# Kernel optimization log

Measured on AMD Instinct MI355X. Metric: run time of the kernel, lower is better.

Reference implementation:

```python
import jax, jax.numpy as jnp
import numpy as np

N_NODES = 100000
N_EDGES = 1600000
IN_C = 128
HID_C = 128   # 2 * out_channels
OUT_C = 64


def gcn_conv(x, row, col, w, W, b, num_nodes):
    """PyG GCNConv: linear transform, add self-loops (weight 1),
    symmetric degree normalization, scatter-sum aggregation, bias."""
    h = x @ W  # [N, C_out]
    loop = jnp.arange(num_nodes, dtype=row.dtype)
    r = jnp.concatenate([row, loop])
    c = jnp.concatenate([col, loop])
    ew = jnp.concatenate([w, jnp.ones((num_nodes,), dtype=w.dtype)])
    deg = jax.ops.segment_sum(ew, c, num_segments=num_nodes)
    dinv = jnp.where(deg > 0, jax.lax.rsqrt(deg), 0.0)
    norm = dinv[r] * ew * dinv[c]            # [E+N]
    msg = h[r] * norm[:, None]               # [E+N, C_out] gather
    out = jax.ops.segment_sum(msg, c, num_segments=num_nodes)
    return out + b


def setup_inputs() -> dict:
    key = jax.random.key(0)
    k1, k2, k3, k4, k5, k6, k7, k8 = jax.random.split(key, 8)
    x = jax.random.normal(k1, (N_NODES, IN_C), dtype=jnp.float32)
    edge_index = jax.random.randint(k2, (2, N_EDGES), 0, N_NODES, dtype=jnp.int64)
    edge_weight = jax.random.uniform(k3, (N_EDGES,), dtype=jnp.float32)
    s1 = float(np.sqrt(6.0 / (IN_C + HID_C)))
    s2 = float(np.sqrt(6.0 / (HID_C + OUT_C)))
    W1 = jax.random.uniform(k4, (IN_C, HID_C), minval=-s1, maxval=s1, dtype=jnp.float32)
    b1 = jnp.zeros((HID_C,), dtype=jnp.float32)
    W2 = jax.random.uniform(k5, (HID_C, OUT_C), minval=-s2, maxval=s2, dtype=jnp.float32)
    b2 = jnp.zeros((OUT_C,), dtype=jnp.float32)
    return {"x": x, "edge_index": edge_index, "edge_weight": edge_weight,
            "W1": W1, "b1": b1, "W2": W2, "b2": b2}


def reference(x, edge_index, edge_weight, W1, b1, W2, b2):
    row, col = edge_index[0], edge_index[1]
    n = x.shape[0]
    h = jax.nn.relu(gcn_conv(x, row, col, edge_weight, W1, b1, n))
    h = jax.nn.relu(gcn_conv(h, row, col, edge_weight, W2, b2, n))
    return h
```

## Files before the change

kernel.cpp:

```cpp
#include <hip/hip_runtime.h>

#define TPB 256

typedef unsigned int uint32;
typedef unsigned short ushort_t;
typedef __attribute__((ext_vector_type(8))) short bf16x8;
typedef __attribute__((ext_vector_type(4))) float f32x4;

constexpr int NB = 256;
constexpr int B1 = 256;

__device__ __forceinline__ uint32 pack_bf16x2(float a, float b) {
  uint32 ua = __float_as_uint(a), ub = __float_as_uint(b);
  ua += 0x7FFFu + ((ua >> 16) & 1u);
  ub += 0x7FFFu + ((ub >> 16) & 1u);
  return (ua >> 16) | (ub & 0xFFFF0000u);
}
__device__ __forceinline__ ushort_t bf16_of(float a) {
  uint32 u = __float_as_uint(a);
  u += 0x7FFFu + ((u >> 16) & 1u);
  return (ushort_t)(u >> 16);
}
__device__ __forceinline__ float bf16_lo(uint32 u) { return __uint_as_float(u << 16); }
__device__ __forceinline__ float bf16_hi(uint32 u) { return __uint_as_float(u & 0xFFFF0000u); }
__device__ __forceinline__ int edge_src(uint32 e) { return (int)(e >> 15); }
__device__ __forceinline__ float edge_w(uint32 e) { return __uint_as_float((e & 0x7FFFu) << 16); }

__global__ __launch_bounds__(256) void rx_hist(const int* __restrict__ col,
                                               int* __restrict__ blockhist, int e, int chunk,
                                               const float* __restrict__ W1, ushort_t* __restrict__ Wt1,
                                               const float* __restrict__ W2, ushort_t* __restrict__ Wt2) {
  __shared__ int h[NB];
  int tid = threadIdx.x, blk = blockIdx.x;
  h[tid] = 0;
  __syncthreads();
  int s = blk * chunk, t = min(e, s + chunk);
  for (int i = s + tid; i < t; i += 256) atomicAdd(&h[col[i] & 255], 1);
  int gtid = blk * 256 + tid;
  if (gtid < 128 * 128) {
    int k = gtid >> 7, m = gtid & 127;
    Wt1[m * 128 + k] = bf16_of(W1[gtid]);
  } else if (gtid < 128 * 128 + 128 * 64) {
    int j = gtid - 128 * 128;
    int k = j >> 6, m = j & 63;
    Wt2[m * 128 + k] = bf16_of(W2[j]);
  }
  __syncthreads();
  blockhist[tid * B1 + blk] = h[tid];
}

__global__ __launch_bounds__(256) void k_scan1(int* __restrict__ a, int* __restrict__ bsum, int n) {
  __shared__ int s[256];
  int tid = threadIdx.x;
  int base = blockIdx.x * 1024 + tid * 4;
  int v0 = 0, v1 = 0, v2 = 0, v3 = 0;
  if (base + 0 < n) v0 = a[base + 0];
  if (base + 1 < n) v1 = a[base + 1];
  if (base + 2 < n) v2 = a[base + 2];
  if (base + 3 < n) v3 = a[base + 3];
  int tsum = v0 + v1 + v2 + v3;
  s[tid] = tsum;
  __syncthreads();
  for (int off = 1; off < 256; off <<= 1) {
    int t = (tid >= off) ? s[tid - off] : 0;
    __syncthreads();
    s[tid] += t;
    __syncthreads();
  }
  if (tid == 255) bsum[blockIdx.x] = s[255];
  int e0 = s[tid] - tsum;
  int e1 = e0 + v0, e2 = e1 + v1, e3 = e2 + v2;
  if (base + 0 < n) a[base + 0] = e0;
  if (base + 1 < n) a[base + 1] = e1;
  if (base + 2 < n) a[base + 2] = e2;
  if (base + 3 < n) a[base + 3] = e3;
}

__global__ __launch_bounds__(256) void k_scan2(int* __restrict__ bsum, int nb) {
  __shared__ int s[256];
  int tid = threadIdx.x;
  int v = (tid < nb) ? bsum[tid] : 0;
  s[tid] = v;
  __syncthreads();
  for (int off = 1; off < 256; off <<= 1) {
    int t = (tid >= off) ? s[tid - off] : 0;
    __syncthreads();
    s[tid] += t;
    __syncthreads();
  }
  if (tid < nb) bsum[tid] = s[tid] - v;
}

__global__ __launch_bounds__(256) void rx_scatter1(const int* __restrict__ row,
                                                   const int* __restrict__ col,
                                                   const float* __restrict__ w,
                                                   const int* __restrict__ scanned,
                                                   const int* __restrict__ bsum,
                                                   int2* __restrict__ rec, int e, int chunk) {
  __shared__ int cur[NB];
  int tid = threadIdx.x, blk = blockIdx.x;
  int idx = tid * B1 + blk;
  cur[tid] = scanned[idx] + bsum[idx >> 10];
  __syncthreads();
  int s = blk * chunk, t = min(e, s + chunk);
  for (int i = s + tid; i < t; i += 256) {
    int c = col[i];
    int p = atomicAdd(&cur[c & 255], 1);
    rec[p] = make_int2(row[i] | ((c >> 8) << 20), __float_as_int(w[i]));
  }
}

__global__ __launch_bounds__(256) void rx_build(const int2* __restrict__ rec,
                                                const int* __restrict__ scanned,
                                                const int* __restrict__ bsum,
                                                int2* __restrict__ nodeRange,
                                                float* __restrict__ dinv,
                                                uint32* __restrict__ edges, int n, int e) {
  constexpr int NH = 512;
  __shared__ int cnt[NH];
  __shared__ int pref[NH];
  __shared__ int cur[NH];
  __shared__ float dw[NH];
  __shared__ int ssum[256];
  int tid = threadIdx.x, lo = blockIdx.x;
  int si = lo * B1;
  int s = scanned[si] + bsum[si >> 10];
  int t;
  if (lo == NB - 1) t = e;
  else {
    int ti = (lo + 1) * B1;
    t = scanned[ti] + bsum[ti >> 10];
  }
  cnt[tid] = 0; cnt[tid + 256] = 0;
  dw[tid] = 0.f; dw[tid + 256] = 0.f;
  __syncthreads();
  for (int i = s + tid; i < t; i += 256) {
    int2 r = rec[i];
    int hi = ((uint32)r.x) >> 20;
    atomicAdd(&cnt[hi], 1);
    atomicAdd(&dw[hi], __int_as_float(r.y));
  }
  __syncthreads();
  int a0 = cnt[2 * tid], a1 = cnt[2 * tid + 1];
  int sum2 = a0 + a1;
  ssum[tid] = sum2;
  __syncthreads();
  for (int off = 1; off < 256; off <<= 1) {
    int v = (tid >= off) ? ssum[tid - off] : 0;
    __syncthreads();
    ssum[tid] += v;
    __syncthreads();
  }
  int excl = ssum[tid] - sum2;
  pref[2 * tid] = excl;
  pref[2 * tid + 1] = excl + a0;
  __syncthreads();
#pragma unroll
  for (int k = 0; k < 2; ++k) {
    int hi = tid + k * 256;
    int node = (hi << 8) | lo;
    cur[hi] = s + pref[hi];
    if (node < n) {
      nodeRange[node] = make_int2(s + pref[hi], cnt[hi]);
      dinv[node] = rsqrtf(1.0f + dw[hi]);
    }
  }
  __syncthreads();
  for (int i = s + tid; i < t; i += 256) {
    int2 r = rec[i];
    int hi = ((uint32)r.x) >> 20;
    int p = atomicAdd(&cur[hi], 1);
    uint32 src = (uint32)(r.x & 0x1FFFF);
    uint32 wb = (uint32)bf16_of(__int_as_float(r.y)) & 0x7FFFu;
    edges[p] = (src << 15) | wb;
  }
}

template <int M, bool XF32>
__global__ __launch_bounds__(256) void k_gemm_mfma(
    const void* __restrict__ Xv, const ushort_t* __restrict__ Wt,
    const float* __restrict__ dinv, uint32* __restrict__ Hb, int n) {
  __shared__ __align__(16) char smem[16384 + M * 256];
  char* Xs = smem;
  char* Ws = smem + 16384;
  const int tid = threadIdx.x;
  const int lane = tid & 63;
  const int w = tid >> 6;
  const int row0 = blockIdx.x * 64;

  {
    const uint4* src = (const uint4*)Wt;
    for (int idx = tid; idx < M * 16; idx += 256) {
      int r = idx >> 4, g = idx & 15;
      uint4 v = src[idx];
      *(uint4*)(Ws + ((r << 8) | ((g << 4) ^ ((r & 7) << 4)))) = v;
    }
  }
  if constexpr (XF32) {
    const float4* src = (const float4*)Xv;
    for (int idx = tid; idx < 64 * 16; idx += 256) {
      int r = idx >> 4, g = idx & 15;
      int grow = row0 + r;
      float4 va = make_float4(0.f, 0.f, 0.f, 0.f), vb = va;
      if (grow < n) {
        va = src[(size_t)grow * 32 + g * 2];
        vb = src[(size_t)grow * 32 + g * 2 + 1];
      }
      uint4 p;
      p.x = pack_bf16x2(va.x, va.y);
      p.y = pack_bf16x2(va.z, va.w);
      p.z = pack_bf16x2(vb.x, vb.y);
      p.w = pack_bf16x2(vb.z, vb.w);
      *(uint4*)(Xs + ((r << 8) | ((g << 4) ^ ((r & 7) << 4)))) = p;
    }
  } else {
    const uint4* src = (const uint4*)Xv;
    for (int idx = tid; idx < 64 * 16; idx += 256) {
      int r = idx >> 4, g = idx & 15;
      int grow = row0 + r;
      uint4 v = make_uint4(0u, 0u, 0u, 0u);
      if (grow < n) v = src[(size_t)grow * 16 + g];
      *(uint4*)(Xs + ((r << 8) | ((g << 4) ^ ((r & 7) << 4)))) = v;
    }
  }
  __syncthreads();

  constexpr int CT = M / 16;
  f32x4 acc[CT];
#pragma unroll
  for (int c = 0; c < CT; ++c) acc[c] = (f32x4){0.f, 0.f, 0.f, 0.f};

  const int arow = (w << 4) | (lane & 15);
  const int kb0 = (lane >> 4) << 4;
#pragma unroll
  for (int ks = 0; ks < 4; ++ks) {
    int kbyte = ks * 64 + kb0;
    bf16x8 a = *(const bf16x8*)(Xs + ((arow << 8) | (kbyte ^ ((arow & 7) << 4))));
#pragma unroll
    for (int c = 0; c < CT; ++c) {
      int brow = c * 16 + (lane & 15);
      bf16x8 b = *(const bf16x8*)(Ws + ((brow << 8) | (kbyte ^ ((brow & 7) << 4))));
      acc[c] = __builtin_amdgcn_mfma_f32_16x16x32_bf16(a, b, acc[c], 0, 0, 0);
    }
  }
  __syncthreads();

  ushort_t* Cs = (ushort_t*)smem;
  const int rbase = (w << 4) | ((lane >> 4) << 2);
  float dv[4];
#pragma unroll
  for (int r = 0; r < 4; ++r) {
    int g = row0 + rbase + r;
    dv[r] = (g < n) ? dinv[g] : 0.f;
  }
#pragma unroll
  for (int c = 0; c < CT; ++c) {
    int col = c * 16 + (lane & 15);
#pragma unroll
    for (int r = 0; r < 4; ++r)
      Cs[(rbase + r) * 132 + col] = bf16_of(acc[c][r] * dv[r]);
  }
  __syncthreads();
  constexpr int G2 = M / 4;
  uint2* dst = (uint2*)Hb;
  for (int idx = tid; idx < 64 * G2; idx += 256) {
    int r = idx / G2, g = idx % G2;
    int grow = row0 + r;
    if (grow < n)
      dst[(size_t)grow * G2 + g] = *(const uint2*)((const char*)Cs + r * 264 + g * 8);
  }
}

template <int C>
__global__ __launch_bounds__(TPB) void k_agg(
    const uint32* __restrict__ hsb, const uint32* __restrict__ edges,
    const int2* __restrict__ nodeRange, const float* __restrict__ dinv,
    const float* __restrict__ bias, void* __restrict__ out, int n) {
  __shared__ uint32 ebuf[TPB / 64][64];
  int node = (blockIdx.x * TPB + threadIdx.x) >> 6;
  if (node >= n) return;
  node = __builtin_amdgcn_readfirstlane(node);
  int lane = threadIdx.x & 63;
  int wv = (threadIdx.x >> 6) & (TPB / 64 - 1);
  int2 nr = nodeRange[node];
  int s0 = nr.x, cnt = nr.y;
  int nLds = min(cnt, 64);
  float di = dinv[node];

  if (lane < nLds)
    ebuf[wv][lane] = __builtin_nontemporal_load(edges + s0 + lane);

  if constexpr (C == 128) {
    int g = lane >> 4;
    int gl = lane & 15;
    const uint4* h4 = (const uint4*)hsb;
    float a0, a1, a2, a3, a4, a5, a6, a7;
    if (g == 0) {
      uint4 u = h4[(size_t)node * 16 + gl];
      a0 = bf16_lo(u.x); a1 = bf16_hi(u.x); a2 = bf16_lo(u.y); a3 = bf16_hi(u.y);
      a4 = bf16_lo(u.z); a5 = bf16_hi(u.z); a6 = bf16_lo(u.w); a7 = bf16_hi(u.w);
    } else {
      a0 = a1 = a2 = a3 = a4 = a5 = a6 = a7 = 0.f;
    }
    int k = g;
    for (; k + 12 < nLds; k += 16) {
      uint32 e0 = ebuf[wv][k], e1 = ebuf[wv][k + 4], e2 = ebuf[wv][k + 8], e3 = ebuf[wv][k + 12];
      uint4 v0 = h4[(size_t)edge_src(e0) * 16 + gl];
      uint4 v1 = h4[(size_t)edge_src(e1) * 16 + gl];
      uint4 v2 = h4[(size_t)edge_src(e2) * 16 + gl];
      uint4 v3 = h4[(size_t)edge_src(e3) * 16 + gl];
      float w0 = edge_w(e0), w1 = edge_w(e1), w2 = edge_w(e2), w3 = edge_w(e3);
      a0 = fmaf(bf16_lo(v0.x), w0, a0); a1 = fmaf(bf16_hi(v0.x), w0, a1);
      a2 = fmaf(bf16_lo(v0.y), w0, a2); a3 = fmaf(bf16_hi(v0.y), w0, a3);
      a4 = fmaf(bf16_lo(v0.z), w0, a4); a5 = fmaf(bf16_hi(v0.z), w0, a5);
      a6 = fmaf(bf16_lo(v0.w), w0, a6); a7 = fmaf(bf16_hi(v0.w), w0, a7);
      a0 = fmaf(bf16_lo(v1.x), w1, a0); a1 = fmaf(bf16_hi(v1.x), w1, a1);
      a2 = fmaf(bf16_lo(v1.y), w1, a2); a3 = fmaf(bf16_hi(v1.y), w1, a3);
      a4 = fmaf(bf16_lo(v1.z), w1, a4); a5 = fmaf(bf16_hi(v1.z), w1, a5);
      a6 = fmaf(bf16_lo(v1.w), w1, a6); a7 = fmaf(bf16_hi(v1.w), w1, a7);
      a0 = fmaf(bf16_lo(v2.x), w2, a0); a1 = fmaf(bf16_hi(v2.x), w2, a1);
      a2 = fmaf(bf16_lo(v2.y), w2, a2); a3 = fmaf(bf16_hi(v2.y), w2, a3);
      a4 = fmaf(bf16_lo(v2.z), w2, a4); a5 = fmaf(bf16_hi(v2.z), w2, a5);
      a6 = fmaf(bf16_lo(v2.w), w2, a6); a7 = fmaf(bf16_hi(v2.w), w2, a7);
      a0 = fmaf(bf16_lo(v3.x), w3, a0); a1 = fmaf(bf16_hi(v3.x), w3, a1);
      a2 = fmaf(bf16_lo(v3.y), w3, a2); a3 = fmaf(bf16_hi(v3.y), w3, a3);
      a4 = fmaf(bf16_lo(v3.z), w3, a4); a5 = fmaf(bf16_hi(v3.z), w3, a5);
      a6 = fmaf(bf16_lo(v3.w), w3, a6); a7 = fmaf(bf16_hi(v3.w), w3, a7);
    }
    for (; k < nLds; k += 4) {
      uint32 e0 = ebuf[wv][k];
      uint4 v0 = h4[(size_t)edge_src(e0) * 16 + gl];
      float w0 = edge_w(e0);
      a0 = fmaf(bf16_lo(v0.x), w0, a0); a1 = fmaf(bf16_hi(v0.x), w0, a1);
      a2 = fmaf(bf16_lo(v0.y), w0, a2); a3 = fmaf(bf16_hi(v0.y), w0, a3);
      a4 = fmaf(bf16_lo(v0.z), w0, a4); a5 = fmaf(bf16_hi(v0.z), w0, a5);
      a6 = fmaf(bf16_lo(v0.w), w0, a6); a7 = fmaf(bf16_hi(v0.w), w0, a7);
    }
    for (int kk = s0 + 64 + g; kk < s0 + cnt; kk += 4) {
      uint32 e0 = edges[kk];
      uint4 v0 = h4[(size_t)edge_src(e0) * 16 + gl];
      float w0 = edge_w(e0);
      a0 = fmaf(bf16_lo(v0.x), w0, a0); a1 = fmaf(bf16_hi(v0.x), w0, a1);
      a2 = fmaf(bf16_lo(v0.y), w0, a2); a3 = fmaf(bf16_hi(v0.y), w0, a3);
      a4 = fmaf(bf16_lo(v0.z), w0, a4); a5 = fmaf(bf16_hi(v0.z), w0, a5);
      a6 = fmaf(bf16_lo(v0.w), w0, a6); a7 = fmaf(bf16_hi(v0.w), w0, a7);
    }
    a0 += __shfl_xor(a0, 16); a1 += __shfl_xor(a1, 16);
    a2 += __shfl_xor(a2, 16); a3 += __shfl_xor(a3, 16);
    a4 += __shfl_xor(a4, 16); a5 += __shfl_xor(a5, 16);
    a6 += __shfl_xor(a6, 16); a7 += __shfl_xor(a7, 16);
    a0 += __shfl_xor(a0, 32); a1 += __shfl_xor(a1, 32);
    a2 += __shfl_xor(a2, 32); a3 += __shfl_xor(a3, 32);
    a4 += __shfl_xor(a4, 32); a5 += __shfl_xor(a5, 32);
    a6 += __shfl_xor(a6, 32); a7 += __shfl_xor(a7, 32);
    if (g == 0) {
      float4 bb0 = ((const float4*)bias)[gl * 2];
      float4 bb1 = ((const float4*)bias)[gl * 2 + 1];
      uint4 ob;
      ob.x = pack_bf16x2(fmaxf(fmaf(a0, di, bb0.x), 0.f), fmaxf(fmaf(a1, di, bb0.y), 0.f));
      ob.y = pack_bf16x2(fmaxf(fmaf(a2, di, bb0.z), 0.f), fmaxf(fmaf(a3, di, bb0.w), 0.f));
      ob.z = pack_bf16x2(fmaxf(fmaf(a4, di, bb1.x), 0.f), fmaxf(fmaf(a5, di, bb1.y), 0.f));
      ob.w = pack_bf16x2(fmaxf(fmaf(a6, di, bb1.z), 0.f), fmaxf(fmaf(a7, di, bb1.w), 0.f));
      ((uint4*)out)[(size_t)node * 16 + gl] = ob;
    }
  } else {
    int g = lane >> 3;
    int gl = lane & 7;
    const uint4* h4 = (const uint4*)hsb;
    float a0, a1, a2, a3, a4, a5, a6, a7;
    if (g == 0) {
      uint4 u = h4[(size_t)node * 8 + gl];
      a0 = bf16_lo(u.x); a1 = bf16_hi(u.x); a2 = bf16_lo(u.y); a3 = bf16_hi(u.y);
      a4 = bf16_lo(u.z); a5 = bf16_hi(u.z); a6 = bf16_lo(u.w); a7 = bf16_hi(u.w);
    } else {
      a0 = a1 = a2 = a3 = a4 = a5 = a6 = a7 = 0.f;
    }
    int k = g;
    for (; k + 8 < nLds; k += 16) {
      uint32 e0 = ebuf[wv][k], e1 = ebuf[wv][k + 8];
      uint4 v0 = h4[(size_t)edge_src(e0) * 8 + gl];
      uint4 v1 = h4[(size_t)edge_src(e1) * 8 + gl];
      float w0 = edge_w(e0), w1 = edge_w(e1);
      a0 = fmaf(bf16_lo(v0.x), w0, a0); a1 = fmaf(bf16_hi(v0.x), w0, a1);
      a2 = fmaf(bf16_lo(v0.y), w0, a2); a3 = fmaf(bf16_hi(v0.y), w0, a3);
      a4 = fmaf(bf16_lo(v0.z), w0, a4); a5 = fmaf(bf16_hi(v0.z), w0, a5);
      a6 = fmaf(bf16_lo(v0.w), w0, a6); a7 = fmaf(bf16_hi(v0.w), w0, a7);
      a0 = fmaf(bf16_lo(v1.x), w1, a0); a1 = fmaf(bf16_hi(v1.x), w1, a1);
      a2 = fmaf(bf16_lo(v1.y), w1, a2); a3 = fmaf(bf16_hi(v1.y), w1, a3);
      a4 = fmaf(bf16_lo(v1.z), w1, a4); a5 = fmaf(bf16_hi(v1.z), w1, a5);
      a6 = fmaf(bf16_lo(v1.w), w1, a6); a7 = fmaf(bf16_hi(v1.w), w1, a7);
    }
    for (; k < nLds; k += 8) {
      uint32 e0 = ebuf[wv][k];
      uint4 v0 = h4[(size_t)edge_src(e0) * 8 + gl];
      float w0 = edge_w(e0);
      a0 = fmaf(bf16_lo(v0.x), w0, a0); a1 = fmaf(bf16_hi(v0.x), w0, a1);
      a2 = fmaf(bf16_lo(v0.y), w0, a2); a3 = fmaf(bf16_hi(v0.y), w0, a3);
      a4 = fmaf(bf16_lo(v0.z), w0, a4); a5 = fmaf(bf16_hi(v0.z), w0, a5);
      a6 = fmaf(bf16_lo(v0.w), w0, a6); a7 = fmaf(bf16_hi(v0.w), w0, a7);
    }
    for (int kk = s0 + 64 + g; kk < s0 + cnt; kk += 8) {
      uint32 e0 = edges[kk];
      uint4 v0 = h4[(size_t)edge_src(e0) * 8 + gl];
      float w0 = edge_w(e0);
      a0 = fmaf(bf16_lo(v0.x), w0, a0); a1 = fmaf(bf16_hi(v0.x), w0, a1);
      a2 = fmaf(bf16_lo(v0.y), w0, a2); a3 = fmaf(bf16_hi(v0.y), w0, a3);
      a4 = fmaf(bf16_lo(v0.z), w0, a4); a5 = fmaf(bf16_hi(v0.z), w0, a5);
      a6 = fmaf(bf16_lo(v0.w), w0, a6); a7 = fmaf(bf16_hi(v0.w), w0, a7);
    }
    a0 += __shfl_xor(a0, 8);  a1 += __shfl_xor(a1, 8);
    a2 += __shfl_xor(a2, 8);  a3 += __shfl_xor(a3, 8);
    a4 += __shfl_xor(a4, 8);  a5 += __shfl_xor(a5, 8);
    a6 += __shfl_xor(a6, 8);  a7 += __shfl_xor(a7, 8);
    a0 += __shfl_xor(a0, 16); a1 += __shfl_xor(a1, 16);
    a2 += __shfl_xor(a2, 16); a3 += __shfl_xor(a3, 16);
    a4 += __shfl_xor(a4, 16); a5 += __shfl_xor(a5, 16);
    a6 += __shfl_xor(a6, 16); a7 += __shfl_xor(a7, 16);
    a0 += __shfl_xor(a0, 32); a1 += __shfl_xor(a1, 32);
    a2 += __shfl_xor(a2, 32); a3 += __shfl_xor(a3, 32);
    a4 += __shfl_xor(a4, 32); a5 += __shfl_xor(a5, 32);
    a6 += __shfl_xor(a6, 32); a7 += __shfl_xor(a7, 32);
    if (g == 0) {
      float4 bb0 = ((const float4*)bias)[gl * 2];
      float4 bb1 = ((const float4*)bias)[gl * 2 + 1];
      float4 o0, o1;
      o0.x = fmaxf(fmaf(a0, di, bb0.x), 0.f);
      o0.y = fmaxf(fmaf(a1, di, bb0.y), 0.f);
      o0.z = fmaxf(fmaf(a2, di, bb0.z), 0.f);
      o0.w = fmaxf(fmaf(a3, di, bb0.w), 0.f);
      o1.x = fmaxf(fmaf(a4, di, bb1.x), 0.f);
      o1.y = fmaxf(fmaf(a5, di, bb1.y), 0.f);
      o1.z = fmaxf(fmaf(a6, di, bb1.z), 0.f);
      o1.w = fmaxf(fmaf(a7, di, bb1.w), 0.f);
      ((float4*)out)[(size_t)node * 16 + gl * 2] = o0;
      ((float4*)out)[(size_t)node * 16 + gl * 2 + 1] = o1;
    }
  }
}

extern "C" void kernel_launch(void* const* d_in, const int* in_sizes, int n_in,
                              void* d_out, int out_size, void* d_ws, size_t ws_size,
                              hipStream_t stream) {
  const float* x  = (const float*)d_in[0];
  const int*   ei = (const int*)d_in[1];
  const float* ew = (const float*)d_in[2];
  const float* W1 = (const float*)d_in[3];
  const float* b1 = (const float*)d_in[4];
  const float* W2 = (const float*)d_in[5];
  const float* b2 = (const float*)d_in[6];
  float* out = (float*)d_out;

  constexpr int IN_C = 128, HID = 128, OUTC = 64;
  const int n = in_sizes[0] / IN_C;
  const int e = in_sizes[2];
  const int* rowp = ei;
  const int* colp = ei + e;

  auto cdiv = [](long a, long b) { return (int)((a + b - 1) / b); };
  auto align = [](size_t v) { return (v + 255) & ~(size_t)255; };

  char* ws = (char*)d_ws;
  size_t o = 0;
  int*      blockhist = (int*)(ws + o);     o = align(o + (size_t)NB * B1 * 4);
  int*      bsum      = (int*)(ws + o);     o = align(o + 4096);
  float*    dinv      = (float*)(ws + o);   o = align(o + (size_t)n * 4);
  int2*     nodeRange = (int2*)(ws + o);    o = align(o + (size_t)n * 8);
  ushort_t* Wt1       = (ushort_t*)(ws + o); o = align(o + (size_t)HID * IN_C * 2);
  ushort_t* Wt2       = (ushort_t*)(ws + o); o = align(o + (size_t)OUTC * HID * 2);
  int2*     rec       = (int2*)(ws + o);    o = align(o + (size_t)e * 8);
  uint32*   edges     = (uint32*)(ws + o);  o = align(o + (size_t)e * 4);
  uint32*   hs1b      = (uint32*)(ws + o);  o = align(o + (size_t)n * (HID / 2) * 4);
  uint32*   o1b       = (uint32*)(ws + o);  o = align(o + (size_t)n * (HID / 2) * 4);
  uint32*   hs2b      = hs1b;

  const int chunk = cdiv(e, B1);
  const int nscan = NB * B1;

  rx_hist<<<B1, 256, 0, stream>>>(colp, blockhist, e, chunk, W1, Wt1, W2, Wt2);
  k_scan1<<<nscan / 1024, 256, 0, stream>>>(blockhist, bsum, nscan);
  k_scan2<<<1, 256, 0, stream>>>(bsum, nscan / 1024);
  rx_scatter1<<<B1, 256, 0, stream>>>(rowp, colp, ew, blockhist, bsum, rec, e, chunk);
  rx_build<<<NB, 256, 0, stream>>>(rec, blockhist, bsum, nodeRange, dinv, edges, n, e);

  k_gemm_mfma<HID, true><<<cdiv(n, 64), 256, 0, stream>>>(x, Wt1, dinv, hs1b, n);
  k_agg<HID><<<cdiv(n, 4), TPB, 0, stream>>>(hs1b, edges, nodeRange, dinv, b1, o1b, n);

  k_gemm_mfma<OUTC, false><<<cdiv(n, 64), 256, 0, stream>>>(o1b, Wt2, dinv, hs2b, n);
  k_agg<OUTC><<<cdiv(n, 4), TPB, 0, stream>>>(hs2b, edges, nodeRange, dinv, b2, out, n);
}
```

Before: 200.1 us.

## Quantize transformed node features to per-row int8 for gather aggregation

```diff
diff --git a/kernel.cpp b/kernel.cpp
--- a/kernel.cpp
+++ b/kernel.cpp
@@ -25,11 +25,16 @@
 __device__ __forceinline__ float bf16_hi(uint32 u) { return __uint_as_float(u & 0xFFFF0000u); }
 __device__ __forceinline__ int edge_src(uint32 e) { return (int)(e >> 15); }
 __device__ __forceinline__ float edge_w(uint32 e) { return __uint_as_float((e & 0x7FFFu) << 16); }
+__device__ __forceinline__ float ubf0(uint32 u) { return (float)(u & 0xFFu); }
+__device__ __forceinline__ float ubf1(uint32 u) { return (float)((u >> 8) & 0xFFu); }
+__device__ __forceinline__ float ubf2(uint32 u) { return (float)((u >> 16) & 0xFFu); }
+__device__ __forceinline__ float ubf3(uint32 u) { return (float)((u >> 24) & 0xFFu); }
 
 __global__ __launch_bounds__(256) void rx_hist(const int* __restrict__ col,
                                                int* __restrict__ blockhist, int e, int chunk,
                                                const float* __restrict__ W1, ushort_t* __restrict__ Wt1,
-                                               const float* __restrict__ W2, ushort_t* __restrict__ Wt2) {
+                                               const float* __restrict__ W2, ushort_t* __restrict__ Wt2,
+                                               const float* __restrict__ b1, float* __restrict__ b1p) {
   __shared__ int h[NB];
   int tid = threadIdx.x, blk = blockIdx.x;
   h[tid] = 0;
@@ -43,7 +48,11 @@
   } else if (gtid < 128 * 128 + 128 * 64) {
     int j = gtid - 128 * 128;
     int k = j >> 6, m = j & 63;
-    Wt2[m * 128 + k] = bf16_of(W2[j]);
+    int kp = ((k & 15) << 3) | (k >> 4);
+    Wt2[m * 128 + kp] = bf16_of(W2[j]);
+  } else if (gtid < 128 * 128 + 128 * 64 + 128) {
+    int p = gtid - (128 * 128 + 128 * 64);
+    b1p[p] = b1[16 * (p & 7) + (p >> 3)];
   }
   __syncthreads();
   blockhist[tid * B1 + blk] = h[tid];
@@ -176,10 +185,11 @@
   }
 }
 
-template <int M, bool XF32>
-__global__ __launch_bounds__(256) void k_gemm_mfma(
+template <int M, bool XF32, bool SWZ>
+__global__ __launch_bounds__(256) void k_gemm_q(
     const void* __restrict__ Xv, const ushort_t* __restrict__ Wt,
-    const float* __restrict__ dinv, uint32* __restrict__ Hb, int n) {
+    const float* __restrict__ dinv, unsigned char* __restrict__ Hb8,
+    float* __restrict__ sc, int n) {
   __shared__ __align__(16) char smem[16384 + M * 256];
   char* Xs = smem;
   char* Ws = smem + 16384;
@@ -245,196 +255,271 @@
   }
   __syncthreads();
 
-  ushort_t* Cs = (ushort_t*)smem;
+  const int gl = lane & 15;
   const int rbase = (w << 4) | ((lane >> 4) << 2);
-  float dv[4];
+  float mx[4] = {0.f, 0.f, 0.f, 0.f};
 #pragma unroll
   for (int r = 0; r < 4; ++r) {
     int g = row0 + rbase + r;
-    dv[r] = (g < n) ? dinv[g] : 0.f;
-  }
-#pragma unroll
-  for (int c = 0; c < CT; ++c) {
-    int col = c * 16 + (lane & 15);
-#pragma unroll
-    for (int r = 0; r < 4; ++r)
-      Cs[(rbase + r) * 132 + col] = bf16_of(acc[c][r] * dv[r]);
-  }
-  __syncthreads();
-  constexpr int G2 = M / 4;
-  uint2* dst = (uint2*)Hb;
-  for (int idx = tid; idx < 64 * G2; idx += 256) {
-    int r = idx / G2, g = idx % G2;
-    int grow = row0 + r;
-    if (grow < n)
-      dst[(size_t)grow * G2 + g] = *(const uint2*)((const char*)Cs + r * 264 + g * 8);
-  }
-}
-
-template <int C>
-__global__ __launch_bounds__(TPB) void k_agg(
-    const uint32* __restrict__ hsb, const uint32* __restrict__ edges,
-    const int2* __restrict__ nodeRange, const float* __restrict__ dinv,
-    const float* __restrict__ bias, void* __restrict__ out, int n) {
+    float dv = (g < n) ? dinv[g] : 0.f;
+#pragma unroll
+    for (int c = 0; c < CT; ++c) {
+      acc[c][r] *= dv;
+      mx[r] = fmaxf(mx[r], fabsf(acc[c][r]));
+    }
+  }
+#pragma unroll
+  for (int off = 1; off < 16; off <<= 1) {
+#pragma unroll
+    for (int r = 0; r < 4; ++r) mx[r] = fmaxf(mx[r], __shfl_xor(mx[r], off));
+  }
+  float inv[4];
+#pragma unroll
+  for (int r = 0; r < 4; ++r) {
+    inv[r] = (mx[r] > 1e-30f) ? 127.0f / mx[r] : 0.f;
+    int g = row0 + rbase + r;
+    if (g < n && gl == 0) sc[g] = mx[r] * (1.0f / 127.0f);
+  }
+
+  if constexpr (SWZ) {
+#pragma unroll
+    for (int r = 0; r < 4; ++r) {
+      int g = row0 + rbase + r;
+      if (g >= n) continue;
+      uint32 lo = 0, hi = 0;
+#pragma unroll
+      for (int c = 0; c < 4; ++c) {
+        uint32 q = (uint32)((int)rintf(acc[c][r] * inv[r]) + 128);
+        lo |= q << (8 * c);
+      }
+#pragma unroll
+      for (int c = 4; c < 8; ++c) {
+        uint32 q = (uint32)((int)rintf(acc[c][r] * inv[r]) + 128);
+        hi |= q << (8 * (c - 4));
+      }
+      ((uint2*)Hb8)[(size_t)g * 16 + gl] = make_uint2(lo, hi);
+    }
+  } else {
+    unsigned char* Cs = (unsigned char*)smem;
+#pragma unroll
+    for (int r = 0; r < 4; ++r) {
+#pragma unroll
+      for (int c = 0; c < CT; ++c) {
+        int q = (int)rintf(acc[c][r] * inv[r]) + 128;
+        Cs[(rbase + r) * 68 + c * 16 + gl] = (unsigned char)q;
+      }
+    }
+    __syncthreads();
+    for (int idx = tid; idx < 64 * (M / 4); idx += 256) {
+      int r = idx / (M / 4), g = idx % (M / 4);
+      int grow = row0 + r;
+      if (grow < n)
+        ((uint32*)Hb8)[(size_t)grow * (M / 4) + g] = *(const uint32*)(Cs + r * 68 + g * 4);
+    }
+  }
+}
+
+__global__ __launch_bounds__(TPB) void k_agg128(
+    const uint2* __restrict__ t8, const float* __restrict__ scs,
+    const uint32* __restrict__ edges, const int2* __restrict__ nodeRange,
+    const float* __restrict__ dinv, const float* __restrict__ b1p,
+    uint4* __restrict__ out, int n) {
   __shared__ uint32 ebuf[TPB / 64][64];
   int node = (blockIdx.x * TPB + threadIdx.x) >> 6;
   if (node >= n) return;
   node = __builtin_amdgcn_readfirstlane(node);
   int lane = threadIdx.x & 63;
   int wv = (threadIdx.x >> 6) & (TPB / 64 - 1);
+  int g = lane >> 4, gl = lane & 15;
   int2 nr = nodeRange[node];
   int s0 = nr.x, cnt = nr.y;
   int nLds = min(cnt, 64);
   float di = dinv[node];
-
-  if (lane < nLds)
-    ebuf[wv][lane] = __builtin_nontemporal_load(edges + s0 + lane);
-
-  if constexpr (C == 128) {
-    int g = lane >> 4;
-    int gl = lane & 15;
-    const uint4* h4 = (const uint4*)hsb;
-    float a0, a1, a2, a3, a4, a5, a6, a7;
-    if (g == 0) {
-      uint4 u = h4[(size_t)node * 16 + gl];
-      a0 = bf16_lo(u.x); a1 = bf16_hi(u.x); a2 = bf16_lo(u.y); a3 = bf16_hi(u.y);
-      a4 = bf16_lo(u.z); a5 = bf16_hi(u.z); a6 = bf16_lo(u.w); a7 = bf16_hi(u.w);
-    } else {
-      a0 = a1 = a2 = a3 = a4 = a5 = a6 = a7 = 0.f;
-    }
-    int k = g;
-    for (; k + 12 < nLds; k += 16) {
-      uint32 e0 = ebuf[wv][k], e1 = ebuf[wv][k + 4], e2 = ebuf[wv][k + 8], e3 = ebuf[wv][k + 12];
-      uint4 v0 = h4[(size_t)edge_src(e0) * 16 + gl];
-      uint4 v1 = h4[(size_t)edge_src(e1) * 16 + gl];
-      uint4 v2 = h4[(size_t)edge_src(e2) * 16 + gl];
-      uint4 v3 = h4[(size_t)edge_src(e3) * 16 + gl];
-      float w0 = edge_w(e0), w1 = edge_w(e1), w2 = edge_w(e2), w3 = edge_w(e3);
-      a0 = fmaf(bf16_lo(v0.x), w0, a0); a1 = fmaf(bf16_hi(v0.x), w0, a1);
-      a2 = fmaf(bf16_lo(v0.y), w0, a2); a3 = fmaf(bf16_hi(v0.y), w0, a3);
-      a4 = fmaf(bf16_lo(v0.z), w0, a4); a5 = fmaf(bf16_hi(v0.z), w0, a5);
-      a6 = fmaf(bf16_lo(v0.w), w0, a6); a7 = fmaf(bf16_hi(v0.w), w0, a7);
-      a0 = fmaf(bf16_lo(v1.x), w1, a0); a1 = fmaf(bf16_hi(v1.x), w1, a1);
-      a2 = fmaf(bf16_lo(v1.y), w1, a2); a3 = fmaf(bf16_hi(v1.y), w1, a3);
-      a4 = fmaf(bf16_lo(v1.z), w1, a4); a5 = fmaf(bf16_hi(v1.z), w1, a5);
-      a6 = fmaf(bf16_lo(v1.w), w1, a6); a7 = fmaf(bf16_hi(v1.w), w1, a7);
-      a0 = fmaf(bf16_lo(v2.x), w2, a0); a1 = fmaf(bf16_hi(v2.x), w2, a1);
-      a2 = fmaf(bf16_lo(v2.y), w2, a2); a3 = fmaf(bf16_hi(v2.y), w2, a3);
-      a4 = fmaf(bf16_lo(v2.z), w2, a4); a5 = fmaf(bf16_hi(v2.z), w2, a5);
-      a6 = fmaf(bf16_lo(v2.w), w2, a6); a7 = fmaf(bf16_hi(v2.w), w2, a7);
-      a0 = fmaf(bf16_lo(v3.x), w3, a0); a1 = fmaf(bf16_hi(v3.x), w3, a1);
-      a2 = fmaf(bf16_lo(v3.y), w3, a2); a3 = fmaf(bf16_hi(v3.y), w3, a3);
-      a4 = fmaf(bf16_lo(v3.z), w3, a4); a5 = fmaf(bf16_hi(v3.z), w3, a5);
-      a6 = fmaf(bf16_lo(v3.w), w3, a6); a7 = fmaf(bf16_hi(v3.w), w3, a7);
-    }
-    for (; k < nLds; k += 4) {
-      uint32 e0 = ebuf[wv][k];
-      uint4 v0 = h4[(size_t)edge_src(e0) * 16 + gl];
-      float w0 = edge_w(e0);
-      a0 = fmaf(bf16_lo(v0.x), w0, a0); a1 = fmaf(bf16_hi(v0.x), w0, a1);
-      a2 = fmaf(bf16_lo(v0.y), w0, a2); a3 = fmaf(bf16_hi(v0.y), w0, a3);
-      a4 = fmaf(bf16_lo(v0.z), w0, a4); a5 = fmaf(bf16_hi(v0.z), w0, a5);
-      a6 = fmaf(bf16_lo(v0.w), w0, a6); a7 = fmaf(bf16_hi(v0.w), w0, a7);
-    }
-    for (int kk = s0 + 64 + g; kk < s0 + cnt; kk += 4) {
-      uint32 e0 = edges[kk];
-      uint4 v0 = h4[(size_t)edge_src(e0) * 16 + gl];
-      float w0 = edge_w(e0);
-      a0 = fmaf(bf16_lo(v0.x), w0, a0); a1 = fmaf(bf16_hi(v0.x), w0, a1);
-      a2 = fmaf(bf16_lo(v0.y), w0, a2); a3 = fmaf(bf16_hi(v0.y), w0, a3);
-      a4 = fmaf(bf16_lo(v0.z), w0, a4); a5 = fmaf(bf16_hi(v0.z), w0, a5);
-      a6 = fmaf(bf16_lo(v0.w), w0, a6); a7 = fmaf(bf16_hi(v0.w), w0, a7);
-    }
-    a0 += __shfl_xor(a0, 16); a1 += __shfl_xor(a1, 16);
-    a2 += __shfl_xor(a2, 16); a3 += __shfl_xor(a3, 16);
-    a4 += __shfl_xor(a4, 16); a5 += __shfl_xor(a5, 16);
-    a6 += __shfl_xor(a6, 16); a7 += __shfl_xor(a7, 16);
-    a0 += __shfl_xor(a0, 32); a1 += __shfl_xor(a1, 32);
-    a2 += __shfl_xor(a2, 32); a3 += __shfl_xor(a3, 32);
-    a4 += __shfl_xor(a4, 32); a5 += __shfl_xor(a5, 32);
-    a6 += __shfl_xor(a6, 32); a7 += __shfl_xor(a7, 32);
-    if (g == 0) {
-      float4 bb0 = ((const float4*)bias)[gl * 2];
-      float4 bb1 = ((const float4*)bias)[gl * 2 + 1];
-      uint4 ob;
-      ob.x = pack_bf16x2(fmaxf(fmaf(a0, di, bb0.x), 0.f), fmaxf(fmaf(a1, di, bb0.y), 0.f));
-      ob.y = pack_bf16x2(fmaxf(fmaf(a2, di, bb0.z), 0.f), fmaxf(fmaf(a3, di, bb0.w), 0.f));
-      ob.z = pack_bf16x2(fmaxf(fmaf(a4, di, bb1.x), 0.f), fmaxf(fmaf(a5, di, bb1.y), 0.f));
-      ob.w = pack_bf16x2(fmaxf(fmaf(a6, di, bb1.z), 0.f), fmaxf(fmaf(a7, di, bb1.w), 0.f));
-      ((uint4*)out)[(size_t)node * 16 + gl] = ob;
-    }
+  if (lane < nLds) ebuf[wv][lane] = __builtin_nontemporal_load(edges + s0 + lane);
+
+  float a0, a1, a2, a3, a4, a5, a6, a7, beta;
+  if (g == 0) {
+    uint2 u = t8[(size_t)node * 16 + gl];
+    float al = scs[node];
+    beta = al;
+    a0 = ubf0(u.x) * al; a1 = ubf1(u.x) * al; a2 = ubf2(u.x) * al; a3 = ubf3(u.x) * al;
+    a4 = ubf0(u.y) * al; a5 = ubf1(u.y) * al; a6 = ubf2(u.y) * al; a7 = ubf3(u.y) * al;
   } else {
-    int g = lane >> 3;
-    int gl = lane & 7;
-    const uint4* h4 = (const uint4*)hsb;
-    float a0, a1, a2, a3, a4, a5, a6, a7;
-    if (g == 0) {
-      uint4 u = h4[(size_t)node * 8 + gl];
-      a0 = bf16_lo(u.x); a1 = bf16_hi(u.x); a2 = bf16_lo(u.y); a3 = bf16_hi(u.y);
-      a4 = bf16_lo(u.z); a5 = bf16_hi(u.z); a6 = bf16_lo(u.w); a7 = bf16_hi(u.w);
-    } else {
-      a0 = a1 = a2 = a3 = a4 = a5 = a6 = a7 = 0.f;
-    }
-    int k = g;
-    for (; k + 8 < nLds; k += 16) {
-      uint32 e0 = ebuf[wv][k], e1 = ebuf[wv][k + 8];
-      uint4 v0 = h4[(size_t)edge_src(e0) * 8 + gl];
-      uint4 v1 = h4[(size_t)edge_src(e1) * 8 + gl];
-      float w0 = edge_w(e0), w1 = edge_w(e1);
-      a0 = fmaf(bf16_lo(v0.x), w0, a0); a1 = fmaf(bf16_hi(v0.x), w0, a1);
-      a2 = fmaf(bf16_lo(v0.y), w0, a2); a3 = fmaf(bf16_hi(v0.y), w0, a3);
-      a4 = fmaf(bf16_lo(v0.z), w0, a4); a5 = fmaf(bf16_hi(v0.z), w0, a5);
-      a6 = fmaf(bf16_lo(v0.w), w0, a6); a7 = fmaf(bf16_hi(v0.w), w0, a7);
-      a0 = fmaf(bf16_lo(v1.x), w1, a0); a1 = fmaf(bf16_hi(v1.x), w1, a1);
-      a2 = fmaf(bf16_lo(v1.y), w1, a2); a3 = fmaf(bf16_hi(v1.y), w1, a3);
-      a4 = fmaf(bf16_lo(v1.z), w1, a4); a5 = fmaf(bf16_hi(v1.z), w1, a5);
-      a6 = fmaf(bf16_lo(v1.w), w1, a6); a7 = fmaf(bf16_hi(v1.w), w1, a7);
-    }
-    for (; k < nLds; k += 8) {
-      uint32 e0 = ebuf[wv][k];
-      uint4 v0 = h4[(size_t)edge_src(e0) * 8 + gl];
-      float w0 = edge_w(e0);
-      a0 = fmaf(bf16_lo(v0.x), w0, a0); a1 = fmaf(bf16_hi(v0.x), w0, a1);
-      a2 = fmaf(bf16_lo(v0.y), w0, a2); a3 = fmaf(bf16_hi(v0.y), w0, a3);
-      a4 = fmaf(bf16_lo(v0.z), w0, a4); a5 = fmaf(bf16_hi(v0.z), w0, a5);
-      a6 = fmaf(bf16_lo(v0.w), w0, a6); a7 = fmaf(bf16_hi(v0.w), w0, a7);
-    }
-    for (int kk = s0 + 64 + g; kk < s0 + cnt; kk += 8) {
-      uint32 e0 = edges[kk];
-      uint4 v0 = h4[(size_t)edge_src(e0) * 8 + gl];
-      float w0 = edge_w(e0);
-      a0 = fmaf(bf16_lo(v0.x), w0, a0); a1 = fmaf(bf16_hi(v0.x), w0, a1);
-      a2 = fmaf(bf16_lo(v0.y), w0, a2); a3 = fmaf(bf16_hi(v0.y), w0, a3);
-      a4 = fmaf(bf16_lo(v0.z), w0, a4); a5 = fmaf(bf16_hi(v0.z), w0, a5);
-      a6 = fmaf(bf16_lo(v0.w), w0, a6); a7 = fmaf(bf16_hi(v0.w), w0, a7);
-    }
-    a0 += __shfl_xor(a0, 8);  a1 += __shfl_xor(a1, 8);
-    a2 += __shfl_xor(a2, 8);  a3 += __shfl_xor(a3, 8);
-    a4 += __shfl_xor(a4, 8);  a5 += __shfl_xor(a5, 8);
-    a6 += __shfl_xor(a6, 8);  a7 += __shfl_xor(a7, 8);
-    a0 += __shfl_xor(a0, 16); a1 += __shfl_xor(a1, 16);
-    a2 += __shfl_xor(a2, 16); a3 += __shfl_xor(a3, 16);
-    a4 += __shfl_xor(a4, 16); a5 += __shfl_xor(a5, 16);
-    a6 += __shfl_xor(a6, 16); a7 += __shfl_xor(a7, 16);
-    a0 += __shfl_xor(a0, 32); a1 += __shfl_xor(a1, 32);
-    a2 += __shfl_xor(a2, 32); a3 += __shfl_xor(a3, 32);
-    a4 += __shfl_xor(a4, 32); a5 += __shfl_xor(a5, 32);
-    a6 += __shfl_xor(a6, 32); a7 += __shfl_xor(a7, 32);
-    if (g == 0) {
-      float4 bb0 = ((const float4*)bias)[gl * 2];
-      float4 bb1 = ((const float4*)bias)[gl * 2 + 1];
-      float4 o0, o1;
-      o0.x = fmaxf(fmaf(a0, di, bb0.x), 0.f);
-      o0.y = fmaxf(fmaf(a1, di, bb0.y), 0.f);
-      o0.z = fmaxf(fmaf(a2, di, bb0.z), 0.f);
-      o0.w = fmaxf(fmaf(a3, di, bb0.w), 0.f);
-      o1.x = fmaxf(fmaf(a4, di, bb1.x), 0.f);
-      o1.y = fmaxf(fmaf(a5, di, bb1.y), 0.f);
-      o1.z = fmaxf(fmaf(a6, di, bb1.z), 0.f);
-      o1.w = fmaxf(fmaf(a7, di, bb1.w), 0.f);
-      ((float4*)out)[(size_t)node * 16 + gl * 2] = o0;
-      ((float4*)out)[(size_t)node * 16 + gl * 2 + 1] = o1;
-    }
+    beta = 0.f;
+    a0 = a1 = a2 = a3 = a4 = a5 = a6 = a7 = 0.f;
+  }
+  int k = g;
+  for (; k + 12 < nLds; k += 16) {
+    uint32 e0 = ebuf[wv][k], e1 = ebuf[wv][k + 4], e2 = ebuf[wv][k + 8], e3 = ebuf[wv][k + 12];
+    int r0 = edge_src(e0), r1 = edge_src(e1), r2 = edge_src(e2), r3 = edge_src(e3);
+    uint2 v0 = t8[(size_t)r0 * 16 + gl];
+    uint2 v1 = t8[(size_t)r1 * 16 + gl];
+    uint2 v2 = t8[(size_t)r2 * 16 + gl];
+    uint2 v3 = t8[(size_t)r3 * 16 + gl];
+    float al0 = edge_w(e0) * scs[r0], al1 = edge_w(e1) * scs[r1];
+    float al2 = edge_w(e2) * scs[r2], al3 = edge_w(e3) * scs[r3];
+    beta += (al0 + al1) + (al2 + al3);
+    a0 = fmaf(ubf0(v0.x), al0, a0); a1 = fmaf(ubf1(v0.x), al0, a1);
+    a2 = fmaf(ubf2(v0.x), al0, a2); a3 = fmaf(ubf3(v0.x), al0, a3);
+    a4 = fmaf(ubf0(v0.y), al0, a4); a5 = fmaf(ubf1(v0.y), al0, a5);
+    a6 = fmaf(ubf2(v0.y), al0, a6); a7 = fmaf(ubf3(v0.y), al0, a7);
+    a0 = fmaf(ubf0(v1.x), al1, a0); a1 = fmaf(ubf1(v1.x), al1, a1);
+    a2 = fmaf(ubf2(v1.x), al1, a2); a3 = fmaf(ubf3(v1.x), al1, a3);
+    a4 = fmaf(ubf0(v1.y), al1, a4); a5 = fmaf(ubf1(v1.y), al1, a5);
+    a6 = fmaf(ubf2(v1.y), al1, a6); a7 = fmaf(ubf3(v1.y), al1, a7);
+    a0 = fmaf(ubf0(v2.x), al2, a0); a1 = fmaf(ubf1(v2.x), al2, a1);
+    a2 = fmaf(ubf2(v2.x), al2, a2); a3 = fmaf(ubf3(v2.x), al2, a3);
+    a4 = fmaf(ubf0(v2.y), al2, a4); a5 = fmaf(ubf1(v2.y), al2, a5);
+    a6 = fmaf(ubf2(v2.y), al2, a6); a7 = fmaf(ubf3(v2.y), al2, a7);
+    a0 = fmaf(ubf0(v3.x), al3, a0); a1 = fmaf(ubf1(v3.x), al3, a1);
+    a2 = fmaf(ubf2(v3.x), al3, a2); a3 = fmaf(ubf3(v3.x), al3, a3);
+    a4 = fmaf(ubf0(v3.y), al3, a4); a5 = fmaf(ubf1(v3.y), al3, a5);
+    a6 = fmaf(ubf2(v3.y), al3, a6); a7 = fmaf(ubf3(v3.y), al3, a7);
+  }
+  for (; k < nLds; k += 4) {
+    uint32 e0 = ebuf[wv][k];
+    int r0 = edge_src(e0);
+    uint2 v0 = t8[(size_t)r0 * 16 + gl];
+    float al0 = edge_w(e0) * scs[r0];
+    beta += al0;
+    a0 = fmaf(ubf0(v0.x), al0, a0); a1 = fmaf(ubf1(v0.x), al0, a1);
+    a2 = fmaf(ubf2(v0.x), al0, a2); a3 = fmaf(ubf3(v0.x), al0, a3);
+    a4 = fmaf(ubf0(v0.y), al0, a4); a5 = fmaf(ubf1(v0.y), al0, a5);
+    a6 = fmaf(ubf2(v0.y), al0, a6); a7 = fmaf(ubf3(v0.y), al0, a7);
+  }
+  for (int kk = s0 + 64 + g; kk < s0 + cnt; kk += 4) {
+    uint32 e0 = edges[kk];
+    int r0 = edge_src(e0);
+    uint2 v0 = t8[(size_t)r0 * 16 + gl];
+    float al0 = edge_w(e0) * scs[r0];
+    beta += al0;
+    a0 = fmaf(ubf0(v0.x), al0, a0); a1 = fmaf(ubf1(v0.x), al0, a1);
+    a2 = fmaf(ubf2(v0.x), al0, a2); a3 = fmaf(ubf3(v0.x), al0, a3);
+    a4 = fmaf(ubf0(v0.y), al0, a4); a5 = fmaf(ubf1(v0.y), al0, a5);
+    a6 = fmaf(ubf2(v0.y), al0, a6); a7 = fmaf(ubf3(v0.y), al0, a7);
+  }
+  a0 += __shfl_xor(a0, 16); a1 += __shfl_xor(a1, 16);
+  a2 += __shfl_xor(a2, 16); a3 += __shfl_xor(a3, 16);
+  a4 += __shfl_xor(a4, 16); a5 += __shfl_xor(a5, 16);
+  a6 += __shfl_xor(a6, 16); a7 += __shfl_xor(a7, 16);
+  beta += __shfl_xor(beta, 16);
+  a0 += __shfl_xor(a0, 32); a1 += __shfl_xor(a1, 32);
+  a2 += __shfl_xor(a2, 32); a3 += __shfl_xor(a3, 32);
+  a4 += __shfl_xor(a4, 32); a5 += __shfl_xor(a5, 32);
+  a6 += __shfl_xor(a6, 32); a7 += __shfl_xor(a7, 32);
+  beta += __shfl_xor(beta, 32);
+  if (g == 0) {
+    float corr = 128.0f * beta;
+    float4 bb0 = ((const float4*)b1p)[gl * 2];
+    float4 bb1 = ((const float4*)b1p)[gl * 2 + 1];
+    float o0 = fmaxf(fmaf(a0 - corr, di, bb0.x), 0.f);
+    float o1 = fmaxf(fmaf(a1 - corr, di, bb0.y), 0.f);
+    float o2 = fmaxf(fmaf(a2 - corr, di, bb0.z), 0.f);
+    float o3 = fmaxf(fmaf(a3 - corr, di, bb0.w), 0.f);
+    float o4 = fmaxf(fmaf(a4 - corr, di, bb1.x), 0.f);
+    float o5 = fmaxf(fmaf(a5 - corr, di, bb1.y), 0.f);
+    float o6 = fmaxf(fmaf(a6 - corr, di, bb1.z), 0.f);
+    float o7 = fmaxf(fmaf(a7 - corr, di, bb1.w), 0.f);
+    uint4 ob;
+    ob.x = pack_bf16x2(o0, o1);
+    ob.y = pack_bf16x2(o2, o3);
+    ob.z = pack_bf16x2(o4, o5);
+    ob.w = pack_bf16x2(o6, o7);
+    out[(size_t)node * 16 + gl] = ob;
+  }
+}
+
+__global__ __launch_bounds__(TPB) void k_agg64(
+    const uint2* __restrict__ t8, const float* __restrict__ scs,
+    const uint32* __restrict__ edges, const int2* __restrict__ nodeRange,
+    const float* __restrict__ dinv, const float* __restrict__ bias,
+    float4* __restrict__ out, int n) {
+  __shared__ uint32 ebuf[TPB / 64][64];
+  int node = (blockIdx.x * TPB + threadIdx.x) >> 6;
+  if (node >= n) return;
+  node = __builtin_amdgcn_readfirstlane(node);
+  int lane = threadIdx.x & 63;
+  int wv = (threadIdx.x >> 6) & (TPB / 64 - 1);
+  int g = lane >> 3, gl = lane & 7;
+  int2 nr = nodeRange[node];
+  int s0 = nr.x, cnt = nr.y;
+  int nLds = min(cnt, 64);
+  float di = dinv[node];
+  if (lane < nLds) ebuf[wv][lane] = __builtin_nontemporal_load(edges + s0 + lane);
+
+  float a0, a1, a2, a3, a4, a5, a6, a7, beta;
+  if (g == 0) {
+    uint2 u = t8[(size_t)node * 8 + gl];
+    float al = scs[node];
+    beta = al;
+    a0 = ubf0(u.x) * al; a1 = ubf1(u.x) * al; a2 = ubf2(u.x) * al; a3 = ubf3(u.x) * al;
+    a4 = ubf0(u.y) * al; a5 = ubf1(u.y) * al; a6 = ubf2(u.y) * al; a7 = ubf3(u.y) * al;
+  } else {
+    beta = 0.f;
+    a0 = a1 = a2 = a3 = a4 = a5 = a6 = a7 = 0.f;
+  }
+  int k = g;
+  for (; k + 8 < nLds; k += 16) {
+    uint32 e0 = ebuf[wv][k], e1 = ebuf[wv][k + 8];
+    int r0 = edge_src(e0), r1 = edge_src(e1);
+    uint2 v0 = t8[(size_t)r0 * 8 + gl];
+    uint2 v1 = t8[(size_t)r1 * 8 + gl];
+    float al0 = edge_w(e0) * scs[r0], al1 = edge_w(e1) * scs[r1];
+    beta += al0 + al1;
+    a0 = fmaf(ubf0(v0.x), al0, a0); a1 = fmaf(ubf1(v0.x), al0, a1);
+    a2 = fmaf(ubf2(v0.x), al0, a2); a3 = fmaf(ubf3(v0.x), al0, a3);
+    a4 = fmaf(ubf0(v0.y), al0, a4); a5 = fmaf(ubf1(v0.y), al0, a5);
+    a6 = fmaf(ubf2(v0.y), al0, a6); a7 = fmaf(ubf3(v0.y), al0, a7);
+    a0 = fmaf(ubf0(v1.x), al1, a0); a1 = fmaf(ubf1(v1.x), al1, a1);
+    a2 = fmaf(ubf2(v1.x), al1, a2); a3 = fmaf(ubf3(v1.x), al1, a3);
+    a4 = fmaf(ubf0(v1.y), al1, a4); a5 = fmaf(ubf1(v1.y), al1, a5);
+    a6 = fmaf(ubf2(v1.y), al1, a6); a7 = fmaf(ubf3(v1.y), al1, a7);
+  }
+  for (; k < nLds; k += 8) {
+    uint32 e0 = ebuf[wv][k];
+    int r0 = edge_src(e0);
+    uint2 v0 = t8[(size_t)r0 * 8 + gl];
+    float al0 = edge_w(e0) * scs[r0];
+    beta += al0;
+    a0 = fmaf(ubf0(v0.x), al0, a0); a1 = fmaf(ubf1(v0.x), al0, a1);
+    a2 = fmaf(ubf2(v0.x), al0, a2); a3 = fmaf(ubf3(v0.x), al0, a3);
+    a4 = fmaf(ubf0(v0.y), al0, a4); a5 = fmaf(ubf1(v0.y), al0, a5);
+    a6 = fmaf(ubf2(v0.y), al0, a6); a7 = fmaf(ubf3(v0.y), al0, a7);
+  }
+  for (int kk = s0 + 64 + g; kk < s0 + cnt; kk += 8) {
+    uint32 e0 = edges[kk];
+    int r0 = edge_src(e0);
+    uint2 v0 = t8[(size_t)r0 * 8 + gl];
+    float al0 = edge_w(e0) * scs[r0];
+    beta += al0;
+    a0 = fmaf(ubf0(v0.x), al0, a0); a1 = fmaf(ubf1(v0.x), al0, a1);
+    a2 = fmaf(ubf2(v0.x), al0, a2); a3 = fmaf(ubf3(v0.x), al0, a3);
+    a4 = fmaf(ubf0(v0.y), al0, a4); a5 = fmaf(ubf1(v0.y), al0, a5);
+    a6 = fmaf(ubf2(v0.y), al0, a6); a7 = fmaf(ubf3(v0.y), al0, a7);
+  }
+#pragma unroll
+  for (int off = 8; off <= 32; off <<= 1) {
+    a0 += __shfl_xor(a0, off); a1 += __shfl_xor(a1, off);
+    a2 += __shfl_xor(a2, off); a3 += __shfl_xor(a3, off);
+    a4 += __shfl_xor(a4, off); a5 += __shfl_xor(a5, off);
+    a6 += __shfl_xor(a6, off); a7 += __shfl_xor(a7, off);
+    beta += __shfl_xor(beta, off);
+  }
+  if (g == 0) {
+    float corr = 128.0f * beta;
+    float4 bb0 = ((const float4*)bias)[gl * 2];
+    float4 bb1 = ((const float4*)bias)[gl * 2 + 1];
+    float4 o0, o1;
+    o0.x = fmaxf(fmaf(a0 - corr, di, bb0.x), 0.f);
+    o0.y = fmaxf(fmaf(a1 - corr, di, bb0.y), 0.f);
+    o0.z = fmaxf(fmaf(a2 - corr, di, bb0.z), 0.f);
+    o0.w = fmaxf(fmaf(a3 - corr, di, bb0.w), 0.f);
+    o1.x = fmaxf(fmaf(a4 - corr, di, bb1.x), 0.f);
+    o1.y = fmaxf(fmaf(a5 - corr, di, bb1.y), 0.f);
+    o1.z = fmaxf(fmaf(a6 - corr, di, bb1.z), 0.f);
+    o1.w = fmaxf(fmaf(a7 - corr, di, bb1.w), 0.f);
+    out[(size_t)node * 16 + gl * 2] = o0;
+    out[(size_t)node * 16 + gl * 2 + 1] = o1;
   }
 }
 
@@ -461,30 +546,35 @@
 
   char* ws = (char*)d_ws;
   size_t o = 0;
-  int*      blockhist = (int*)(ws + o);     o = align(o + (size_t)NB * B1 * 4);
-  int*      bsum      = (int*)(ws + o);     o = align(o + 4096);
-  float*    dinv      = (float*)(ws + o);   o = align(o + (size_t)n * 4);
-  int2*     nodeRange = (int2*)(ws + o);    o = align(o + (size_t)n * 8);
+  int*      blockhist = (int*)(ws + o);      o = align(o + (size_t)NB * B1 * 4);
+  int*      bsum      = (int*)(ws + o);      o = align(o + 4096);
+  float*    dinv      = (float*)(ws + o);    o = align(o + (size_t)n * 4);
+  int2*     nodeRange = (int2*)(ws + o);     o = align(o + (size_t)n * 8);
   ushort_t* Wt1       = (ushort_t*)(ws + o); o = align(o + (size_t)HID * IN_C * 2);
   ushort_t* Wt2       = (ushort_t*)(ws + o); o = align(o + (size_t)OUTC * HID * 2);
-  int2*     rec       = (int2*)(ws + o);    o = align(o + (size_t)e * 8);
-  uint32*   edges     = (uint32*)(ws + o);  o = align(o + (size_t)e * 4);
-  uint32*   hs1b      = (uint32*)(ws + o);  o = align(o + (size_t)n * (HID / 2) * 4);
-  uint32*   o1b       = (uint32*)(ws + o);  o = align(o + (size_t)n * (HID / 2) * 4);
-  uint32*   hs2b      = hs1b;
+  float*    b1p       = (float*)(ws + o);    o = align(o + 512);
+  float*    sc1       = (float*)(ws + o);    o = align(o + (size_t)n * 4);
+  float*    sc2       = (float*)(ws + o);    o = align(o + (size_t)n * 4);
+  int2*     rec       = (int2*)(ws + o);     o = align(o + (size_t)e * 8);
+  uint32*   edges     = (uint32*)(ws + o);   o = align(o + (size_t)e * 4);
+  unsigned char* hs1b8 = (unsigned char*)(ws + o); o = align(o + (size_t)n * HID);
+  uint4*    o1b       = (uint4*)(ws + o);    o = align(o + (size_t)n * HID * 2);
+  unsigned char* hs2b8 = hs1b8;
 
   const int chunk = cdiv(e, B1);
   const int nscan = NB * B1;
 
-  rx_hist<<<B1, 256, 0, stream>>>(colp, blockhist, e, chunk, W1, Wt1, W2, Wt2);
+  rx_hist<<<B1, 256, 0, stream>>>(colp, blockhist, e, chunk, W1, Wt1, W2, Wt2, b1, b1p);
   k_scan1<<<nscan / 1024, 256, 0, stream>>>(blockhist, bsum, nscan);
   k_scan2<<<1, 256, 0, stream>>>(bsum, nscan / 1024);
   rx_scatter1<<<B1, 256, 0, stream>>>(rowp, colp, ew, blockhist, bsum, rec, e, chunk);
   rx_build<<<NB, 256, 0, stream>>>(rec, blockhist, bsum, nodeRange, dinv, edges, n, e);
 
-  k_gemm_mfma<HID, true><<<cdiv(n, 64), 256, 0, stream>>>(x, Wt1, dinv, hs1b, n);
-  k_agg<HID><<<cdiv(n, 4), TPB, 0, stream>>>(hs1b, edges, nodeRange, dinv, b1, o1b, n);
-
-  k_gemm_mfma<OUTC, false><<<cdiv(n, 64), 256, 0, stream>>>(o1b, Wt2, dinv, hs2b, n);
-  k_agg<OUTC><<<cdiv(n, 4), TPB, 0, stream>>>(hs2b, edges, nodeRange, dinv, b2, out, n);
-}
+  k_gemm_q<HID, true, true><<<cdiv(n, 64), 256, 0, stream>>>(x, Wt1, dinv, hs1b8, sc1, n);
+  k_agg128<<<cdiv(n, 4), TPB, 0, stream>>>((const uint2*)hs1b8, sc1, edges, nodeRange,
+                                           dinv, b1p, o1b, n);
+
+  k_gemm_q<OUTC, false, false><<<cdiv(n, 64), 256, 0, stream>>>(o1b, Wt2, dinv, hs2b8, sc2, n);
+  k_agg64<<<cdiv(n, 4), TPB, 0, stream>>>((const uint2*)hs2b8, sc2, edges, nodeRange,
+                                          dinv, b2, (float4*)out, n);
+}
```

Measured after the change: 193.9 us. 3.1% less time.
